# Kernel optimization log

Measured on AMD Instinct MI355X. Metric: run time of the kernel, lower is better.

## Reference

```python
import jax, jax.numpy as jnp
import numpy as np

N_ACTORS = 50000
N_EDGES = 800000
D = 128
L = 2
EDGE_IN = 2 * D + 2  # src feat + rel (x,y) + dst feat


def setup_inputs() -> dict:
    key = jax.random.key(0)
    ks = jax.random.split(key, 6)
    actor_features = jax.random.normal(ks[0], (N_ACTORS, D), dtype=jnp.float32)
    edge_dist_rel = jax.random.normal(ks[1], (N_EDGES, 2), dtype=jnp.float32)
    # per-layer learned weights (bias=False in both Linears)
    W_att = jax.random.normal(ks[2], (L, EDGE_IN), dtype=jnp.float32) * 0.05
    W_emb = jax.random.normal(ks[3], (L, D, EDGE_IN), dtype=jnp.float32) * 0.05
    edge_src_idx = jax.random.randint(ks[4], (N_EDGES,), 0, N_ACTORS, dtype=jnp.int32)
    edge_dst_idx = jax.random.randint(ks[5], (N_EDGES,), 0, N_ACTORS, dtype=jnp.int32)
    return {
        "actor_features": actor_features,
        "edge_dist_rel": edge_dist_rel,
        "W_att": W_att,
        "W_emb": W_emb,
        "edge_src_idx": edge_src_idx,
        "edge_dst_idx": edge_dst_idx,
    }


def _scatter_softmax(scores, dst_idx, num_segments):
    # numerically stable softmax over irregular dst groups
    seg_max = jax.ops.segment_max(scores, dst_idx, num_segments=num_segments)
    ex = jnp.exp(scores - seg_max[dst_idx])
    denom = jax.ops.segment_sum(ex, dst_idx, num_segments=num_segments)
    return ex / denom[dst_idx]


def reference(actor_features, edge_dist_rel, W_att, W_emb, edge_src_idx, edge_dst_idx):
    n = actor_features.shape[0]
    feat = actor_features
    for l in range(W_att.shape[0]):  # small fixed number of layers
        # gather per-edge features and build edge inputs [E, 2D+2]
        e_in = jnp.concatenate(
            [feat[edge_src_idx], edge_dist_rel, feat[edge_dst_idx]], axis=-1)
        # edge attention: Linear(edge_in -> 1, no bias) + LeakyReLU(0.2)
        s = jax.nn.leaky_relu(e_in @ W_att[l], negative_slope=0.2)  # [E]
        att = _scatter_softmax(s, edge_dst_idx, n)  # dropout omitted (eval mode)
        # edge embed: Linear(edge_in -> D, no bias)
        emb = e_in @ W_emb[l].T  # [E, D]
        agg = jax.ops.segment_sum(att[:, None] * emb, edge_dst_idx, num_segments=n)
        feat = jax.nn.relu(agg)
    return feat
```

## Files before the change

### kernel.cpp

```cpp
#include <hip/hip_runtime.h>
#include <hip/hip_fp16.h>

#define D 128
#define EDGE_IN 258

typedef __attribute__((ext_vector_type(8))) short bf16x8;
typedef __attribute__((ext_vector_type(4))) float f32x4;

__device__ __forceinline__ float rl_f(float v, int j) {
  return __int_as_float(__builtin_amdgcn_readlane(__float_as_int(v), j));
}
__device__ __forceinline__ int rl_i(int v, int j) {
  return __builtin_amdgcn_readlane(v, j);
}
__device__ __forceinline__ ushort f32_to_bf16(float f) {
  unsigned u = __float_as_uint(f);
  unsigned r = (u + 0x7FFFu + ((u >> 16) & 1u)) >> 16;
  return (ushort)r;
}
__device__ __forceinline__ float bf16_to_f32(ushort h) {
  return __uint_as_float(((unsigned)h) << 16);
}

__global__ void zero_int(int* __restrict__ p, int n) {
  int i = blockIdx.x * blockDim.x + threadIdx.x;
  if (i < n) p[i] = 0;
}

__global__ void hist_kernel(const int* __restrict__ dst, int* __restrict__ deg, int ne) {
  int e = blockIdx.x * blockDim.x + threadIdx.x;
  if (e < ne) atomicAdd(&deg[dst[e]], 1);
}

__global__ __launch_bounds__(256) void scan_part(const int* __restrict__ deg,
                                                 int* __restrict__ bsum, int n) {
  __shared__ int red[256];
  int b = blockIdx.x, tid = threadIdx.x;
  int base = b * 1024 + tid * 4;
  int s = 0;
#pragma unroll
  for (int j = 0; j < 4; j++) { int idx = base + j; if (idx < n) s += deg[idx]; }
  red[tid] = s;
  __syncthreads();
  for (int off = 128; off; off >>= 1) {
    if (tid < off) red[tid] += red[tid + off];
    __syncthreads();
  }
  if (tid == 0) bsum[b] = red[0];
}

__global__ __launch_bounds__(256) void scan_bsums(int* __restrict__ bsum, int nb) {
  __shared__ int part[256];
  int tid = threadIdx.x;
  int v = (tid < nb) ? bsum[tid] : 0;
  part[tid] = v;
  __syncthreads();
  for (int off = 1; off < 256; off <<= 1) {
    int t = (tid >= off) ? part[tid - off] : 0;
    __syncthreads();
    part[tid] += t;
    __syncthreads();
  }
  if (tid < nb) bsum[tid] = (tid == 0) ? 0 : part[tid - 1];
}

__global__ __launch_bounds__(256) void scan_final(const int* __restrict__ deg,
                                                  const int* __restrict__ bsumex,
                                                  int* __restrict__ offs,
                                                  int* __restrict__ cur, int n, int ne) {
  __shared__ int part[256];
  int b = blockIdx.x, tid = threadIdx.x;
  int base = b * 1024 + tid * 4;
  int v[4];
  int s = 0;
#pragma unroll
  for (int j = 0; j < 4; j++) {
    int idx = base + j;
    v[j] = (idx < n) ? deg[idx] : 0;
    s += v[j];
  }
  part[tid] = s;
  __syncthreads();
  for (int off = 1; off < 256; off <<= 1) {
    int t = (tid >= off) ? part[tid - off] : 0;
    __syncthreads();
    part[tid] += t;
    __syncthreads();
  }
  int run = bsumex[b] + ((tid == 0) ? 0 : part[tid - 1]);
#pragma unroll
  for (int j = 0; j < 4; j++) {
    int idx = base + j;
    if (idx < n) { offs[idx] = run; cur[idx] = run; run += v[j]; }
  }
  if (b == 0 && tid == 0) offs[n] = ne;
}

__global__ void scatter_kernel(const int* __restrict__ dst, const int* __restrict__ srcIdx,
                               const float2* __restrict__ rel, int* __restrict__ cur,
                               float4* __restrict__ meta, int ne) {
  int e = blockIdx.x * blockDim.x + threadIdx.x;
  if (e < ne) {
    int p = atomicAdd(&cur[dst[e]], 1);
    float2 r = rel[e];
    meta[p] = make_float4(__int_as_float(srcIdx[e]), r.x, r.y, 0.f);
  }
}

__global__ void prep_weights(const float* __restrict__ W_emb,
                             const float* __restrict__ W_att,
                             ushort* __restrict__ WBhi, ushort* __restrict__ WBlo) {
  int lane = threadIdx.x;
  int kt = blockIdx.x / 9, nt = blockIdx.x % 9;
  int part = blockIdx.y, l = blockIdx.z;
  int off = part ? 130 : 0;
  int g = lane >> 4, nn = lane & 15;
  int n = nt * 16 + nn;
  size_t base = (((size_t)((l * 2 + part) * 4 + kt) * 9 + nt) * 64 + lane) * 8;
#pragma unroll
  for (int e = 0; e < 8; e++) {
    int k = kt * 32 + 8 * g + e;
    float val = 0.f;
    if (nt < 8) val = W_emb[(size_t)(l * D + n) * EDGE_IN + off + k];
    else if (nn == 0) val = W_att[(size_t)l * EDGE_IN + off + k];
    ushort hi = f32_to_bf16(val);
    WBhi[base + e] = hi;
    WBlo[base + e] = f32_to_bf16(val - bf16_to_f32(hi));
  }
}

__global__ void rel_prep(const float* __restrict__ W_emb, float* __restrict__ Wrel) {
  int d = threadIdx.x;
  int c = blockIdx.x;
  int l = blockIdx.y;
  Wrel[(l * 2 + c) * 128 + d] = W_emb[(size_t)(l * D + d) * EDGE_IN + 128 + c];
}

__global__ __launch_bounds__(128) void proj_kernel(
    const float* __restrict__ feat, const ushort* __restrict__ WBhi,
    const ushort* __restrict__ WBlo, __half* __restrict__ Ps16,
    float* __restrict__ Pd, float* __restrict__ a_s, float* __restrict__ a_d,
    int n, int l) {
  __shared__ ushort Ahi[4][64][8];
  __shared__ ushort Alo[4][64][8];
  int i0 = blockIdx.x * 16;
  int tid = threadIdx.x;

  for (int t = tid; t < 512; t += 128) {
    int m = t >> 5;
    int k4 = t & 31;
    int gi = i0 + m;
    float4 v = (gi < n) ? ((const float4*)feat)[(size_t)gi * 32 + k4]
                        : make_float4(0.f, 0.f, 0.f, 0.f);
    int kt = k4 >> 3;
    int lanew = m + 16 * ((k4 >> 1) & 3);
    int eh = (k4 & 1) * 4;
    ushort hx = f32_to_bf16(v.x), hy = f32_to_bf16(v.y);
    ushort hz = f32_to_bf16(v.z), hw = f32_to_bf16(v.w);
    ushort4 h4 = make_ushort4(hx, hy, hz, hw);
    ushort4 l4 = make_ushort4(f32_to_bf16(v.x - bf16_to_f32(hx)),
                              f32_to_bf16(v.y - bf16_to_f32(hy)),
                              f32_to_bf16(v.z - bf16_to_f32(hz)),
                              f32_to_bf16(v.w - bf16_to_f32(hw)));
    *(ushort4*)&Ahi[kt][lanew][eh] = h4;
    *(ushort4*)&Alo[kt][lanew][eh] = l4;
  }
  __syncthreads();

  int w = tid >> 6;
  int lane = tid & 63;

  bf16x8 ah[4], al[4];
#pragma unroll
  for (int kt = 0; kt < 4; kt++) {
    ah[kt] = *(const bf16x8*)&Ahi[kt][lane][0];
    al[kt] = *(const bf16x8*)&Alo[kt][lane][0];
  }

  const ushort* bh = WBhi + (size_t)(l * 2 + w) * 4 * 9 * 64 * 8;
  const ushort* bl = WBlo + (size_t)(l * 2 + w) * 4 * 9 * 64 * 8;

  f32x4 acc[9];
#pragma unroll
  for (int i = 0; i < 9; i++) acc[i] = (f32x4){0.f, 0.f, 0.f, 0.f};

#pragma unroll
  for (int nt = 0; nt < 9; nt++) {
#pragma unroll
    for (int kt = 0; kt < 4; kt++) {
      size_t idx = (((size_t)kt * 9 + nt) * 64 + lane) * 8;
      bf16x8 bhv = *(const bf16x8*)&bh[idx];
      bf16x8 blv = *(const bf16x8*)&bl[idx];
      acc[nt] = __builtin_amdgcn_mfma_f32_16x16x32_bf16(ah[kt], bhv, acc[nt], 0, 0, 0);
      acc[nt] = __builtin_amdgcn_mfma_f32_16x16x32_bf16(al[kt], bhv, acc[nt], 0, 0, 0);
      acc[nt] = __builtin_amdgcn_mfma_f32_16x16x32_bf16(ah[kt], blv, acc[nt], 0, 0, 0);
    }
  }

  int col0 = lane & 15, rowg = lane >> 4;
  if (w == 0) {
#pragma unroll
    for (int nt = 0; nt < 8; nt++)
#pragma unroll
      for (int r = 0; r < 4; r++) {
        int gi = i0 + rowg * 4 + r;
        if (gi < n) Ps16[(size_t)gi * D + nt * 16 + col0] = __float2half(acc[nt][r]);
      }
    if (col0 == 0) {
#pragma unroll
      for (int r = 0; r < 4; r++) {
        int gi = i0 + rowg * 4 + r;
        if (gi < n) a_s[gi] = acc[8][r];
      }
    }
  } else {
#pragma unroll
    for (int nt = 0; nt < 8; nt++)
#pragma unroll
      for (int r = 0; r < 4; r++) {
        int gi = i0 + rowg * 4 + r;
        if (gi < n) Pd[(size_t)gi * D + nt * 16 + col0] = acc[nt][r];
      }
    if (col0 == 0) {
#pragma unroll
      for (int r = 0; r < 4; r++) {
        int gi = i0 + rowg * 4 + r;
        if (gi < n) a_d[gi] = acc[8][r];
      }
    }
  }
}

__global__ __launch_bounds__(256) void edge_kernel(
    const __half2* __restrict__ Ps, const float* __restrict__ Pd,
    const float* __restrict__ a_s, const float* __restrict__ a_d,
    const float4* __restrict__ meta, const int* __restrict__ offs,
    const float* __restrict__ Wrel, const float* __restrict__ W_att,
    float* __restrict__ out, int n, int l) {
  int wid = (blockIdx.x * blockDim.x + threadIdx.x) >> 6;
  if (wid >= n) return;
  int lane = threadIdx.x & 63;
  int d0 = 2 * lane;
  float wax = W_att[(size_t)l * EDGE_IN + 128];
  float way = W_att[(size_t)l * EDGE_IN + 129];
  float ad = a_d[wid];
  int p0 = offs[wid], p1 = offs[wid + 1];
  float m = -1e30f, lsum = 0.f, Sx = 0.f, Sy = 0.f;
  float accx = 0.f, accy = 0.f;
  for (int c0 = p0; c0 < p1; c0 += 64) {
    int cn = min(64, p1 - c0);
    int si = 0;
    float rx = 0.f, ry = 0.f, s = -1e30f;
    if (lane < cn) {
      float4 mt = meta[c0 + lane];
      si = __float_as_int(mt.x);
      rx = mt.y;
      ry = mt.z;
      float sc = a_s[si] + ad + rx * wax + ry * way;
      s = (sc > 0.f) ? sc : 0.2f * sc;
    }
    float cm = s;
#pragma unroll
    for (int o = 32; o; o >>= 1) cm = fmaxf(cm, __shfl_xor(cm, o, 64));
    float mnew = fmaxf(m, cm);
    float corr = __expf(m - mnew);
    float w = (lane < cn) ? __expf(s - mnew) : 0.f;
    float cw = w, cwx = w * rx, cwy = w * ry;
#pragma unroll
    for (int o = 32; o; o >>= 1) {
      cw += __shfl_xor(cw, o, 64);
      cwx += __shfl_xor(cwx, o, 64);
      cwy += __shfl_xor(cwy, o, 64);
    }
    lsum = lsum * corr + cw;
    Sx = Sx * corr + cwx;
    Sy = Sy * corr + cwy;
    accx *= corr;
    accy *= corr;
    m = mnew;
    int j = 0;
    for (; j + 8 <= cn; j += 8) {
      float2 f[8];
      float wj[8];
#pragma unroll
      for (int q = 0; q < 8; q++) {
        int sj = rl_i(si, j + q);
        wj[q] = rl_f(w, j + q);
        f[q] = __half22float2(Ps[(size_t)sj * 64 + lane]);
      }
#pragma unroll
      for (int q = 0; q < 8; q++) {
        accx += wj[q] * f[q].x;
        accy += wj[q] * f[q].y;
      }
    }
    if (j < cn) {
      float2 f[8];
      float wj[8];
      int r = cn - j;
#pragma unroll
      for (int q = 0; q < 8; q++) {
        if (q < r) {
          int sj = rl_i(si, j + q);
          wj[q] = rl_f(w, j + q);
          f[q] = __half22float2(Ps[(size_t)sj * 64 + lane]);
        }
      }
#pragma unroll
      for (int q = 0; q < 8; q++) {
        if (q < r) {
          accx += wj[q] * f[q].x;
          accy += wj[q] * f[q].y;
        }
      }
    }
  }
  float2 o2 = make_float2(0.f, 0.f);
  if (p1 > p0) {
    const float2 wc0 = *(const float2*)&Wrel[(l * 2 + 0) * 128 + d0];
    const float2 wc1 = *(const float2*)&Wrel[(l * 2 + 1) * 128 + d0];
    float inv = 1.0f / lsum;
    float2 pd = *(const float2*)&Pd[(size_t)wid * D + d0];
    accx += Sx * wc0.x + Sy * wc1.x;
    accy += Sx * wc0.y + Sy * wc1.y;
    o2.x = fmaxf(accx * inv + pd.x, 0.f);
    o2.y = fmaxf(accy * inv + pd.y, 0.f);
  }
  *(float2*)&out[(size_t)wid * D + d0] = o2;
}

extern "C" void kernel_launch(void* const* d_in, const int* in_sizes, int n_in,
                              void* d_out, int out_size, void* d_ws, size_t ws_size,
                              hipStream_t stream) {
  const float* actor = (const float*)d_in[0];
  const float* rel   = (const float*)d_in[1];
  const float* W_att = (const float*)d_in[2];
  const float* W_emb = (const float*)d_in[3];
  const int* srcIdx  = (const int*)d_in[4];
  const int* dstIdx  = (const int*)d_in[5];
  int n  = in_sizes[0] / D;
  int ne = in_sizes[4];
  int Lnum = in_sizes[2] / EDGE_IN;
  float* fout_last = (float*)d_out;

  float* ws = (float*)d_ws;
  size_t o = 0;
  float4* meta = (float4*)ws; o += 4 * (size_t)ne;
  size_t wbN = (size_t)Lnum * 2 * 4 * 9 * 64 * 8;
  ushort* WBhi = (ushort*)(ws + o); o += (wbN + 1) / 2;
  ushort* WBlo = (ushort*)(ws + o); o += (wbN + 1) / 2;
  float* Wre = ws + o; o += (size_t)Lnum * 2 * 128;
  float* Pd  = ws + o; o += (size_t)n * D;
  float* a_s = ws + o; o += (size_t)n + 64;
  float* a_d = ws + o; o += (size_t)n + 64;
  __half* Ps16 = (__half*)(ws + o); o += (size_t)n * D / 2;
  int* ibuf = (int*)(ws + o);
  size_t io = 0;
  int* deg  = ibuf + io; io += n + 64;
  int* offs = ibuf + io; io += n + 64;
  int* cur  = ibuf + io; io += n + 64;
  int* bsum = ibuf + io; io += 256;

  int nb = (n + 1023) / 1024;

  zero_int<<<(n + 255) / 256, 256, 0, stream>>>(deg, n);
  hist_kernel<<<(ne + 255) / 256, 256, 0, stream>>>(dstIdx, deg, ne);
  scan_part<<<nb, 256, 0, stream>>>(deg, bsum, n);
  scan_bsums<<<1, 256, 0, stream>>>(bsum, nb);
  scan_final<<<nb, 256, 0, stream>>>(deg, bsum, offs, cur, n, ne);
  scatter_kernel<<<(ne + 255) / 256, 256, 0, stream>>>(dstIdx, srcIdx, (const float2*)rel,
                                                       cur, meta, ne);
  prep_weights<<<dim3(36, 2, Lnum), 64, 0, stream>>>(W_emb, W_att, WBhi, WBlo);
  rel_prep<<<dim3(2, Lnum), 128, 0, stream>>>(W_emb, Wre);

  const float* fin = actor;
  int nt16 = (n + 15) / 16;
  for (int l = 0; l < Lnum; l++) {
    proj_kernel<<<nt16, 128, 0, stream>>>(fin, WBhi, WBlo, Ps16, Pd, a_s, a_d, n, l);
    edge_kernel<<<(n + 3) / 4, 256, 0, stream>>>((const __half2*)Ps16, Pd, a_s, a_d, meta,
                                                 offs, Wre, W_att, fout_last, n, l);
    fin = fout_last;
  }
}
```

Baseline: 349.0 us.

## Pack edge metadata into int2 with half-precision rel coords; batch atomics per thread

Shrinks the per-edge CSR metadata from a 16-byte float4 to an 8-byte int2 holding the source index plus the relative (x,y) stored as half2. This halves the scatter write traffic and the edge_kernel metadata reads. The histogram and scatter kernels now each process four edges per thread with fewer blocks, so several atomics are in flight per thread. Storing rel coords in fp16 loses precision in the attention score and the rel term of the embedding, which could affect accuracy.

```diff
diff --git a/kernel.cpp b/kernel.cpp
--- a/kernel.cpp
+++ b/kernel.cpp
@@ -28,8 +28,12 @@
 }
 
 __global__ void hist_kernel(const int* __restrict__ dst, int* __restrict__ deg, int ne) {
-  int e = blockIdx.x * blockDim.x + threadIdx.x;
-  if (e < ne) atomicAdd(&deg[dst[e]], 1);
+  int base = blockIdx.x * 1024 + threadIdx.x;
+#pragma unroll
+  for (int k = 0; k < 4; k++) {
+    int e = base + k * 256;
+    if (e < ne) atomicAdd(&deg[dst[e]], 1);
+  }
 }
 
 __global__ __launch_bounds__(256) void scan_part(const int* __restrict__ deg,
@@ -98,13 +102,29 @@
 
 __global__ void scatter_kernel(const int* __restrict__ dst, const int* __restrict__ srcIdx,
                                const float2* __restrict__ rel, int* __restrict__ cur,
-                               float4* __restrict__ meta, int ne) {
-  int e = blockIdx.x * blockDim.x + threadIdx.x;
-  if (e < ne) {
-    int p = atomicAdd(&cur[dst[e]], 1);
-    float2 r = rel[e];
-    meta[p] = make_float4(__int_as_float(srcIdx[e]), r.x, r.y, 0.f);
-  }
+                               int2* __restrict__ meta, int ne) {
+  int base = blockIdx.x * 1024 + threadIdx.x;
+  int e[4], p[4];
+  int2 mv[4];
+  int cnt = 0;
+#pragma unroll
+  for (int k = 0; k < 4; k++) {
+    int ek = base + k * 256;
+    if (ek < ne) {
+      float2 r = rel[ek];
+      __half2 h = __floats2half2_rn(r.x, r.y);
+      mv[cnt].x = srcIdx[ek];
+      mv[cnt].y = *(int*)&h;
+      e[cnt] = ek;
+      cnt++;
+    }
+  }
+#pragma unroll
+  for (int k = 0; k < 4; k++)
+    if (k < cnt) p[k] = atomicAdd(&cur[dst[e[k]]], 1);
+#pragma unroll
+  for (int k = 0; k < 4; k++)
+    if (k < cnt) meta[p[k]] = mv[k];
 }
 
 __global__ void prep_weights(const float* __restrict__ W_emb,
@@ -234,7 +254,7 @@
 __global__ __launch_bounds__(256) void edge_kernel(
     const __half2* __restrict__ Ps, const float* __restrict__ Pd,
     const float* __restrict__ a_s, const float* __restrict__ a_d,
-    const float4* __restrict__ meta, const int* __restrict__ offs,
+    const int2* __restrict__ meta, const int* __restrict__ offs,
     const float* __restrict__ Wrel, const float* __restrict__ W_att,
     float* __restrict__ out, int n, int l) {
   int wid = (blockIdx.x * blockDim.x + threadIdx.x) >> 6;
@@ -252,10 +272,11 @@
     int si = 0;
     float rx = 0.f, ry = 0.f, s = -1e30f;
     if (lane < cn) {
-      float4 mt = meta[c0 + lane];
-      si = __float_as_int(mt.x);
-      rx = mt.y;
-      ry = mt.z;
+      int2 mt = meta[c0 + lane];
+      si = mt.x;
+      float2 rr = __half22float2(*(__half2*)&mt.y);
+      rx = rr.x;
+      ry = rr.y;
       float sc = a_s[si] + ad + rx * wax + ry * way;
       s = (sc > 0.f) ? sc : 0.2f * sc;
     }
@@ -345,7 +366,7 @@
 
   float* ws = (float*)d_ws;
   size_t o = 0;
-  float4* meta = (float4*)ws; o += 4 * (size_t)ne;
+  int2* meta = (int2*)ws; o += 2 * (size_t)ne;
   size_t wbN = (size_t)Lnum * 2 * 4 * 9 * 64 * 8;
   ushort* WBhi = (ushort*)(ws + o); o += (wbN + 1) / 2;
   ushort* WBlo = (ushort*)(ws + o); o += (wbN + 1) / 2;
@@ -362,14 +383,14 @@
   int* bsum = ibuf + io; io += 256;
 
   int nb = (n + 1023) / 1024;
+  int nbe = (ne + 1023) / 1024;
 
   zero_int<<<(n + 255) / 256, 256, 0, stream>>>(deg, n);
-  hist_kernel<<<(ne + 255) / 256, 256, 0, stream>>>(dstIdx, deg, ne);
+  hist_kernel<<<nbe, 256, 0, stream>>>(dstIdx, deg, ne);
   scan_part<<<nb, 256, 0, stream>>>(deg, bsum, n);
   scan_bsums<<<1, 256, 0, stream>>>(bsum, nb);
   scan_final<<<nb, 256, 0, stream>>>(deg, bsum, offs, cur, n, ne);
-  scatter_kernel<<<(ne + 255) / 256, 256, 0, stream>>>(dstIdx, srcIdx, (const float2*)rel,
-                                                       cur, meta, ne);
+  scatter_kernel<<<nbe, 256, 0, stream>>>(dstIdx, srcIdx, (const float2*)rel, cur, meta, ne);
   prep_weights<<<dim3(36, 2, Lnum), 64, 0, stream>>>(W_emb, W_att, WBhi, WBlo);
   rel_prep<<<dim3(2, Lnum), 128, 0, stream>>>(W_emb, Wre);
 
```

New measurement: 350.5 us. About the same (+0.4%).
